# Kernel tuning notes

Hardware: AMD Instinct MI355X
Metric: run time of the kernel (lower is better)

The kernel has to match this reference:

```python
import jax, jax.numpy as jnp
import numpy as np

# ---- configuration (mirrors cfg used by the torch module) ----
H = W = 64          # cfg.KEYPOINT.HEATMAP_SIZE
C = 256             # cfg.KEYPOINT.NFEATS
N = 2               # batch (number of view pairs)
S = 32              # cfg.EPIPOLAR.SAMPLESIZE
DS = 4              # cfg.BACKBONE.DOWNSAMPLE
EPS = 1e-3          # self.epsilon


def pix2coord(v):
    # feature-map pixel -> original-image coordinate
    return v * DS + DS / 2.0 - 0.5


def _camera_pair():
    # realistic stereo pair: image is 256x256 (64x64 heatmap * downsample 4)
    K = np.array([[300.0, 0.0, 127.5], [0.0, 300.0, 127.5], [0.0, 0.0, 1.0]])
    P1 = K @ np.hstack([np.eye(3), np.zeros((3, 1))])
    ang = np.deg2rad(15.0)
    R = np.array([[np.cos(ang), 0, np.sin(ang)], [0, 1, 0], [-np.sin(ang), 0, np.cos(ang)]])
    t = np.array([[-0.5], [0.0], [0.1]])
    P2 = K @ np.hstack([R, t])
    return P1.astype(np.float32), P2.astype(np.float32)


def setup_inputs() -> dict:
    key = jax.random.key(0)
    k1, k2 = jax.random.split(key)
    feat1 = jax.random.normal(k1, (N, C, H, W), dtype=jnp.float32)
    feat2 = jax.random.normal(k2, (N, C, H, W), dtype=jnp.float32)
    P1np, P2np = _camera_pair()
    P1 = jnp.asarray(np.stack([P1np] * N))
    P2 = jnp.asarray(np.stack([P2np] * N))
    return {"feat1": feat1, "feat2": feat2, "P1": P1, "P2": P2}


def _fundamental(P1, P2):
    # F = [e2]_x P2 P1^+ ; camera center = null vector of P1
    P1inv = jnp.linalg.pinv(P1)          # 4x3
    _, _, Vt = jnp.linalg.svd(P1)
    Cc = Vt[-1]                          # homogeneous camera center, (4,)
    e2 = P2 @ Cc                         # epipole in view 2, (3,)
    z = jnp.zeros(())
    skew = jnp.stack([jnp.stack([z, -e2[2], e2[1]]),
                      jnp.stack([e2[2], z, -e2[0]]),
                      jnp.stack([-e2[1], e2[0], z])])
    return skew @ (P2 @ P1inv)


def _sample_locs(P1, P2):
    """Epipolar-line sample locations, [S, N, H, W, 2] normalized to [-1,1]."""
    xs = pix2coord(jnp.arange(W, dtype=jnp.float32))
    ys = pix2coord(jnp.arange(H, dtype=jnp.float32))
    xmin, xmax = xs[0], xs[-1]
    ymin, ymax = ys[0], ys[-1]
    gy, gx = jnp.meshgrid(ys, xs, indexing='ij')
    grid = jnp.stack([gx.ravel(), gy.ravel(), jnp.ones(H * W, jnp.float32)])

    F = jax.vmap(_fundamental)(P1, P2)
    lines = jnp.einsum('nij,jp->nip', F, grid)
    a, b, c = lines[:, 0], lines[:, 1], lines[:, 2]
    a_s = jnp.where(jnp.abs(a) < EPS, EPS, a)
    b_s = jnp.where(jnp.abs(b) < EPS, EPS, b)
    # intersections of a*x + b*y + c = 0 with the 4 image borders
    y_at_xmin = -(c + a * xmin) / b_s
    y_at_xmax = -(c + a * xmax) / b_s
    x_at_ymin = -(c + b * ymin) / a_s
    x_at_ymax = -(c + b * ymax) / a_s
    cx = jnp.stack([jnp.full_like(a, xmin), jnp.full_like(a, xmax), x_at_ymin, x_at_ymax], -1)  # N,HW,4
    cy = jnp.stack([y_at_xmin, y_at_xmax, jnp.full_like(a, ymin), jnp.full_like(a, ymax)], -1)
    tol = 1e-2
    valid = (cx >= xmin - tol) & (cx <= xmax + tol) & (cy >= ymin - tol) & (cy <= ymax + tol)
    # invalid -> far out of range (equivalent of self.outrange_tensor);
    # such sample locs fall outside [-1,1] and contribute zeros in grid_sample
    cx = jnp.where(valid, cx, xmin - 10000.0)
    cy = jnp.where(valid, cy, ymin - 10000.0)
    order = jnp.argsort(jnp.logical_not(valid), axis=-1)  # stable: valid candidates first
    pick = order[..., :2]                                 # N,HW,2
    px = jnp.take_along_axis(cx, pick, axis=-1)
    py = jnp.take_along_axis(cy, pick, axis=-1)
    # normalize original-image coords to [-1,1] over the feature grid extent
    nx = (px - xmin) / (xmax - xmin) * 2.0 - 1.0
    ny = (py - ymin) / (ymax - ymin) * 2.0 - 1.0
    start = jnp.stack([nx[..., 0], ny[..., 0]], -1)       # N,HW,2
    end = jnp.stack([nx[..., 1], ny[..., 1]], -1)
    steps = jnp.linspace(0.0, 1.0, S).reshape(S, 1, 1, 1)
    locs = start[None] + steps * (end - start)[None]      # S,N,HW,2
    return locs.reshape(S, N, H, W, 2)


def _grid_sample(img, grid):
    """Bilinear sampling with zeros padding. img [C,H,W], grid [S,H,W,2] -> [S,C,H,W]."""
    gx, gy = grid[..., 0], grid[..., 1]
    x = (gx + 1.0) * 0.5 * (W - 1)
    y = (gy + 1.0) * 0.5 * (H - 1)
    x0 = jnp.floor(x)
    y0 = jnp.floor(y)
    wx = x - x0
    wy = y - y0
    x0i = x0.astype(jnp.int32)
    y0i = y0.astype(jnp.int32)

    def gather(yi, xi, w):
        inb = (yi >= 0) & (yi <= H - 1) & (xi >= 0) & (xi <= W - 1)
        yc = jnp.clip(yi, 0, H - 1)
        xc = jnp.clip(xi, 0, W - 1)
        vals = img[:, yc, xc]                  # C,S,H,W
        return vals * (w * inb)[None]

    out = (gather(y0i, x0i, (1 - wy) * (1 - wx))
           + gather(y0i, x0i + 1, (1 - wy) * wx)
           + gather(y0i + 1, x0i, wy * (1 - wx))
           + gather(y0i + 1, x0i + 1, wy * wx))
    return out.transpose(1, 0, 2, 3)           # S,C,H,W


def reference(feat1, feat2, P1, P2):
    # geometry (torch.no_grad in original)
    locs = jax.lax.stop_gradient(_sample_locs(P1, P2))   # S,N,H,W,2
    locs_n = jnp.transpose(locs, (1, 0, 2, 3, 4))        # N,S,H,W,2
    sampled = jax.vmap(_grid_sample)(feat2, locs_n)      # N,S,C,H,W
    # dot-product similarity + softmax attention over the epipolar samples ('avg')
    sim = jax.nn.softmax(jnp.einsum('nchw,nschw->nshw', feat1, sampled), axis=1)
    out = jnp.einsum('nshw,nschw->nchw', sim, sampled)   # N,C,H,W
    return out
```

## Files before the change

### kernel.cpp

```cpp
#include <hip/hip_runtime.h>
#include <math.h>

#define H 64
#define W 64
#define C 256
#define NB 2
#define SS 32
#define HW (H*W)

typedef __attribute__((ext_vector_type(2))) _Float16 half2v;

__device__ __forceinline__ half2v pk2(float a) {
  return __builtin_bit_cast(half2v, __builtin_amdgcn_cvt_pkrtz(a, a));
}

__device__ void fmat_compute(const float* __restrict__ P1f,
                             const float* __restrict__ P2f,
                             double* __restrict__ Fout, int n) {
  double p1[3][4], p2[3][4];
  for (int i = 0; i < 3; ++i)
    for (int j = 0; j < 4; ++j) {
      p1[i][j] = (double)P1f[n * 12 + i * 4 + j];
      p2[i][j] = (double)P2f[n * 12 + i * 4 + j];
    }
  double A[3][3];
  for (int i = 0; i < 3; ++i)
    for (int j = 0; j < 3; ++j) {
      double s = 0;
      for (int k = 0; k < 4; ++k) s += p1[i][k] * p1[j][k];
      A[i][j] = s;
    }
  double det = A[0][0] * (A[1][1] * A[2][2] - A[1][2] * A[2][1])
             - A[0][1] * (A[1][0] * A[2][2] - A[1][2] * A[2][0])
             + A[0][2] * (A[1][0] * A[2][1] - A[1][1] * A[2][0]);
  double id = 1.0 / det;
  double Ai[3][3];
  Ai[0][0] = (A[1][1] * A[2][2] - A[1][2] * A[2][1]) * id;
  Ai[0][1] = (A[0][2] * A[2][1] - A[0][1] * A[2][2]) * id;
  Ai[0][2] = (A[0][1] * A[1][2] - A[0][2] * A[1][1]) * id;
  Ai[1][0] = (A[1][2] * A[2][0] - A[1][0] * A[2][2]) * id;
  Ai[1][1] = (A[0][0] * A[2][2] - A[0][2] * A[2][0]) * id;
  Ai[1][2] = (A[0][2] * A[1][0] - A[0][0] * A[1][2]) * id;
  Ai[2][0] = (A[1][0] * A[2][1] - A[1][1] * A[2][0]) * id;
  Ai[2][1] = (A[0][1] * A[2][0] - A[0][0] * A[2][1]) * id;
  Ai[2][2] = (A[0][0] * A[1][1] - A[0][1] * A[1][0]) * id;
  double Pi[4][3];
  for (int i = 0; i < 4; ++i)
    for (int j = 0; j < 3; ++j) {
      double s = 0;
      for (int k = 0; k < 3; ++k) s += p1[k][i] * Ai[k][j];
      Pi[i][j] = s;
    }
  double M[3][3];
  for (int i = 0; i < 3; ++i)
    for (int j = 0; j < 3; ++j) {
      double s = 0;
      for (int k = 0; k < 4; ++k) s += p2[i][k] * Pi[k][j];
      M[i][j] = s;
    }
  double nv[4];
  {
    auto det3 = [&](int ca, int cb, int cc) {
      return p1[0][ca] * (p1[1][cb] * p1[2][cc] - p1[1][cc] * p1[2][cb])
           - p1[0][cb] * (p1[1][ca] * p1[2][cc] - p1[1][cc] * p1[2][ca])
           + p1[0][cc] * (p1[1][ca] * p1[2][cb] - p1[1][cb] * p1[2][ca]);
    };
    nv[0] =  det3(1, 2, 3);
    nv[1] = -det3(0, 2, 3);
    nv[2] =  det3(0, 1, 3);
    nv[3] = -det3(0, 1, 2);
  }
  double nn = sqrt(nv[0]*nv[0] + nv[1]*nv[1] + nv[2]*nv[2] + nv[3]*nv[3]);
  for (int i = 0; i < 4; ++i) nv[i] /= nn;
  double e2[3];
  for (int i = 0; i < 3; ++i) {
    double s = 0;
    for (int j = 0; j < 4; ++j) s += p2[i][j] * nv[j];
    e2[i] = s;
  }
  for (int j = 0; j < 3; ++j) {
    Fout[n * 9 + 0 * 3 + j] = -e2[2] * M[1][j] + e2[1] * M[2][j];
    Fout[n * 9 + 1 * 3 + j] =  e2[2] * M[0][j] - e2[0] * M[2][j];
    Fout[n * 9 + 2 * 3 + j] = -e2[1] * M[0][j] + e2[0] * M[1][j];
  }
}

__global__ __launch_bounds__(256) void prep_kernel(
    const float* __restrict__ feat2,
    const float* __restrict__ P1f, const float* __restrict__ P2f,
    _Float16* __restrict__ f2t, double* __restrict__ Fd) {
  __shared__ float tile[32][33];
  const int n  = blockIdx.z;
  const int p0 = blockIdx.x * 32;
  const int c0 = blockIdx.y * 32;
  const int tx = threadIdx.x, ty = threadIdx.y;
  const float* src = feat2 + (size_t)n * (C * HW);
#pragma unroll
  for (int j = 0; j < 4; ++j) {
    int cc = c0 + ty + j * 8;
    tile[ty + j * 8][tx] = src[(size_t)cc * HW + p0 + tx];
  }
  __syncthreads();
  {
    const int tid = ty * 32 + tx;
    const int pp = tid >> 3;
    const int cp = tid & 7;
    _Float16* dst = f2t + (size_t)n * (HW * C) + (size_t)(p0 + pp) * C + c0;
#pragma unroll
    for (int jj = 0; jj < 2; ++jj) {
      const int cc = (cp + jj * 8) * 2;
      half2v h2;
      h2.x = (_Float16)tile[cc][pp];
      h2.y = (_Float16)tile[cc + 1][pp];
      *(half2v*)(dst + cc) = h2;
    }
  }
  if (n == 0 && blockIdx.x == 0 && blockIdx.y == 0) {
    int t = ty * 32 + tx;
    if (t < NB) fmat_compute(P1f, P2f, Fd, t);
  }
}

__device__ __forceinline__ float groupsum32(float v) {
  v += __int_as_float(__builtin_amdgcn_update_dpp(
         0, __float_as_int(v), 0xB1, 0xF, 0xF, true));
  v += __int_as_float(__builtin_amdgcn_update_dpp(
         0, __float_as_int(v), 0x4E, 0xF, 0xF, true));
  v += __int_as_float(__builtin_amdgcn_update_dpp(
         0, __float_as_int(v), 0x124, 0xF, 0xF, true));
  v += __int_as_float(__builtin_amdgcn_update_dpp(
         0, __float_as_int(v), 0x128, 0xF, 0xF, true));
  v += __int_as_float(__builtin_amdgcn_ds_swizzle(
         __float_as_int(v), 0x401F));
  return v;
}

struct Stage {
  uint4 a, b, c, d;
  half2v wa, wb, wc, wd;
};

__global__ __launch_bounds__(256) void epi_main(
    const float* __restrict__ feat1, const _Float16* __restrict__ f2t,
    const double* __restrict__ Fd, float* __restrict__ out) {
  const int tid  = threadIdx.x;
  const int lane = tid & 63;
  const int wv   = tid >> 6;
  const int grp  = lane >> 5;
  const int cl   = lane & 31;
  const int bid  = blockIdx.x;
  const int r    = bid & 7;
  const int k    = bid >> 3;
  const int n    = r >> 2;
  const int sub  = r & 3;
  const int p    = (sub * 128 + k) * 8 + wv * 2 + grp;
  const int h = p >> 6, w = p & (W - 1);
  const int cb = cl * 8;

  float f1r[8];
  {
    const float* f1b = feat1 + ((size_t)n * C + cb) * HW + p;
#pragma unroll
    for (int i = 0; i < 8; ++i) f1r[i] = f1b[(size_t)i * HW];
  }

  const double* Fdp = Fd + n * 9;
  const float F0 = (float)Fdp[0], F1 = (float)Fdp[1], F2 = (float)Fdp[2];
  const float F3 = (float)Fdp[3], F4 = (float)Fdp[4], F5 = (float)Fdp[5];
  const float F6 = (float)Fdp[6], F7 = (float)Fdp[7], F8 = (float)Fdp[8];
  const float X = w * 4.0f + 1.5f;
  const float Y = h * 4.0f + 1.5f;
  const float a = F0 * X + F1 * Y + F2;
  const float b = F3 * X + F4 * Y + F5;
  const float c = F6 * X + F7 * Y + F8;
  const float a_s = (fabsf(a) < 1e-3f) ? 1e-3f : a;
  const float b_s = (fabsf(b) < 1e-3f) ? 1e-3f : b;
  const float xmin = 1.5f, xmax = 253.5f, ymin = 1.5f, ymax = 253.5f, tol = 0.01f;
  float cx[4], cy[4];
  cx[0] = xmin;  cy[0] = -(c + a * xmin) / b_s;
  cx[1] = xmax;  cy[1] = -(c + a * xmax) / b_s;
  cx[2] = -(c + b * ymin) / a_s;  cy[2] = ymin;
  cx[3] = -(c + b * ymax) / a_s;  cy[3] = ymax;
  bool valid[4];
#pragma unroll
  for (int i = 0; i < 4; ++i)
    valid[i] = (cx[i] >= xmin - tol) && (cx[i] <= xmax + tol) &&
               (cy[i] >= ymin - tol) && (cy[i] <= ymax + tol);
#pragma unroll
  for (int i = 0; i < 4; ++i)
    if (!valid[i]) { cx[i] = xmin - 10000.0f; cy[i] = ymin - 10000.0f; }
  int pk0 = -1, pk1 = -1;
#pragma unroll
  for (int i = 0; i < 4; ++i)
    if (valid[i]) { if (pk0 < 0) pk0 = i; else if (pk1 < 0) pk1 = i; }
#pragma unroll
  for (int i = 0; i < 4; ++i)
    if (!valid[i]) { if (pk0 < 0) pk0 = i; else if (pk1 < 0) pk1 = i; }
  const float x0p = (cx[pk0] - 1.5f) * 0.25f;
  const float y0p = (cy[pk0] - 1.5f) * 0.25f;
  const float pdx = (cx[pk1] - 1.5f) * 0.25f - x0p;
  const float pdy = (cy[pk1] - 1.5f) * 0.25f - y0p;

  const _Float16* f2b = f2t + (size_t)n * HW * C + cb;

  float m = -1e30f, l = 0.f;
  half2v acc2[4];
#pragma unroll
  for (int i = 0; i < 4; ++i) acc2[i] = (half2v)(_Float16)0;

  auto issue = [&](int s, Stage& st) {
    const float t = (float)s * (1.0f / 31.0f);
    const float x = fmaf(t, pdx, x0p);
    const float y = fmaf(t, pdy, y0p);
    const float xf = floorf(x), yf = floorf(y);
    const float wx = x - xf, wy = y - yf;
    const int x0 = (int)xf, y0 = (int)yf;
    const bool bx0 = ((unsigned)x0 < W), bx1 = ((unsigned)(x0 + 1) < W);
    const bool by0 = ((unsigned)y0 < H), by1 = ((unsigned)(y0 + 1) < H);
    const int xc0 = min(max(x0, 0), W - 1);
    const int xc1 = min(max(x0 + 1, 0), W - 1);
    const int yc0 = min(max(y0, 0), H - 1);
    const int yc1 = min(max(y0 + 1, 0), H - 1);
    const float u0 = 1.f - wx, v0 = 1.f - wy;
    const float w00 = v0 * u0 * (float)(bx0 & by0);
    const float w01 = v0 * wx * (float)(bx1 & by0);
    const float w10 = wy * u0 * (float)(bx0 & by1);
    const float w11 = wy * wx * (float)(bx1 & by1);
    st.wa = pk2(w00);
    st.wb = pk2(w01);
    st.wc = pk2(w10);
    st.wd = pk2(w11);
    const int r0 = yc0 * W, r1 = yc1 * W;
    st.a = *(const uint4*)(f2b + (r0 + xc0) * C);
    st.b = *(const uint4*)(f2b + (r0 + xc1) * C);
    st.c = *(const uint4*)(f2b + (r1 + xc0) * C);
    st.d = *(const uint4*)(f2b + (r1 + xc1) * C);
  };

  auto process = [&](const Stage& st) {
    half2v q[4];
    {
      const uint* ap = (const uint*)&st.a;
      const uint* bp = (const uint*)&st.b;
      const uint* cp = (const uint*)&st.c;
      const uint* dp = (const uint*)&st.d;
#pragma unroll
      for (int j = 0; j < 4; ++j) {
        half2v qa = __builtin_bit_cast(half2v, ap[j]) * st.wa;
        qa += __builtin_bit_cast(half2v, bp[j]) * st.wb;
        qa += __builtin_bit_cast(half2v, cp[j]) * st.wc;
        qa += __builtin_bit_cast(half2v, dp[j]) * st.wd;
        q[j] = qa;
      }
    }
    float part = 0.f;
#pragma unroll
    for (int j = 0; j < 4; ++j) {
      part = fmaf(f1r[2 * j],     (float)q[j].x, part);
      part = fmaf(f1r[2 * j + 1], (float)q[j].y, part);
    }
    part = groupsum32(part);

    if (__any(part > m + 4.f)) {
      const float mn = fmaxf(m, part);
      const float sc = __expf(m - mn);
      l *= sc;
      const half2v sch = pk2(sc);
#pragma unroll
      for (int i = 0; i < 4; ++i) acc2[i] *= sch;
      m = mn;
    }
    const float e = __expf(part - m);
    l += e;
    const half2v eh = pk2(e);
#pragma unroll
    for (int i = 0; i < 4; ++i) acc2[i] += eh * q[i];
  };

  Stage sA, sB, sC;
  issue(0, sA);
  issue(1, sB);
  for (int k3 = 0; k3 < 30; k3 += 3) {
    issue(k3 + 2, sC);
    process(sA);
    issue(k3 + 3, sA);
    process(sB);
    issue(k3 + 4, sB);
    process(sC);
  }
  process(sA);
  process(sB);

  const float inv = 1.0f / l;
  float* ob = out + (size_t)n * C * HW + (size_t)cb * HW + p;
#pragma unroll
  for (int i = 0; i < 4; ++i) {
    ob[(size_t)(2 * i) * HW]     = (float)acc2[i].x * inv;
    ob[(size_t)(2 * i + 1) * HW] = (float)acc2[i].y * inv;
  }
}

extern "C" void kernel_launch(void* const* d_in, const int* in_sizes, int n_in,
                              void* d_out, int out_size, void* d_ws, size_t ws_size,
                              hipStream_t stream) {
  const float* feat1 = (const float*)d_in[0];
  const float* feat2 = (const float*)d_in[1];
  const float* P1 = (const float*)d_in[2];
  const float* P2 = (const float*)d_in[3];
  float* out = (float*)d_out;

  char* ws = (char*)d_ws;
  _Float16* f2t = (_Float16*)ws;
  double*   Fd  = (double*)(ws + (5u << 20));

  prep_kernel<<<dim3(HW / 32, C / 32, NB), dim3(32, 8), 0, stream>>>(
      feat2, P1, P2, f2t, Fd);
  epi_main<<<NB * HW / 8, 256, 0, stream>>>(feat1, f2t, Fd, out);
}
```

Before: 40.67 us.

## Use fp16 dot2 for similarity and process samples in unrolled pairs

Feat1 values are packed to fp16 pairs so the similarity dot product can use the packed fdot2 instruction instead of per-element float conversions and FMAs. The explicit three-stage software pipeline is replaced by a fully unrolled loop that handles two samples per step, sharing one online-softmax rescale check and one max per pair. This cuts ALU and cross-lane reduction overhead per sample, but feat1 drops to fp16 precision and prefetch depth is left to the compiler, which may raise register pressure or hide less load latency.

```diff
diff --git a/kernel.cpp b/kernel.cpp
--- a/kernel.cpp
+++ b/kernel.cpp
@@ -9,9 +9,21 @@
 #define HW (H*W)
 
 typedef __attribute__((ext_vector_type(2))) _Float16 half2v;
+typedef __attribute__((ext_vector_type(2))) __fp16   fp16x2;
 
 __device__ __forceinline__ half2v pk2(float a) {
   return __builtin_bit_cast(half2v, __builtin_amdgcn_cvt_pkrtz(a, a));
+}
+
+__device__ __forceinline__ float fdot2(half2v a, half2v b, float c) {
+#if __has_builtin(__builtin_amdgcn_fdot2)
+  return __builtin_amdgcn_fdot2(__builtin_bit_cast(fp16x2, a),
+                                __builtin_bit_cast(fp16x2, b), c, false);
+#else
+  c = fmaf((float)a.x, (float)b.x, c);
+  c = fmaf((float)a.y, (float)b.y, c);
+  return c;
+#endif
 }
 
 __device__ void fmat_compute(const float* __restrict__ P1f,
@@ -134,11 +146,6 @@
          __float_as_int(v), 0x401F));
   return v;
 }
-
-struct Stage {
-  uint4 a, b, c, d;
-  half2v wa, wb, wc, wd;
-};
 
 __global__ __launch_bounds__(256) void epi_main(
     const float* __restrict__ feat1, const _Float16* __restrict__ f2t,
@@ -157,11 +164,15 @@
   const int h = p >> 6, w = p & (W - 1);
   const int cb = cl * 8;
 
-  float f1r[8];
+  half2v f1h[4];
   {
     const float* f1b = feat1 + ((size_t)n * C + cb) * HW + p;
 #pragma unroll
-    for (int i = 0; i < 8; ++i) f1r[i] = f1b[(size_t)i * HW];
+    for (int i = 0; i < 4; ++i) {
+      const float lo = f1b[(size_t)(2 * i) * HW];
+      const float hi = f1b[(size_t)(2 * i + 1) * HW];
+      f1h[i] = __builtin_bit_cast(half2v, __builtin_amdgcn_cvt_pkrtz(lo, hi));
+    }
   }
 
   const double* Fdp = Fd + n * 9;
@@ -208,7 +219,8 @@
 #pragma unroll
   for (int i = 0; i < 4; ++i) acc2[i] = (half2v)(_Float16)0;
 
-  auto issue = [&](int s, Stage& st) {
+  auto fetch = [&](int s, uint4& A, uint4& B, uint4& Cc, uint4& D,
+                   half2v& wa, half2v& wb, half2v& wc, half2v& wd) {
     const float t = (float)s * (1.0f / 31.0f);
     const float x = fmaf(t, pdx, x0p);
     const float y = fmaf(t, pdy, y0p);
@@ -222,47 +234,53 @@
     const int yc0 = min(max(y0, 0), H - 1);
     const int yc1 = min(max(y0 + 1, 0), H - 1);
     const float u0 = 1.f - wx, v0 = 1.f - wy;
-    const float w00 = v0 * u0 * (float)(bx0 & by0);
-    const float w01 = v0 * wx * (float)(bx1 & by0);
-    const float w10 = wy * u0 * (float)(bx0 & by1);
-    const float w11 = wy * wx * (float)(bx1 & by1);
-    st.wa = pk2(w00);
-    st.wb = pk2(w01);
-    st.wc = pk2(w10);
-    st.wd = pk2(w11);
+    wa = pk2(v0 * u0 * (float)(bx0 & by0));
+    wb = pk2(v0 * wx * (float)(bx1 & by0));
+    wc = pk2(wy * u0 * (float)(bx0 & by1));
+    wd = pk2(wy * wx * (float)(bx1 & by1));
     const int r0 = yc0 * W, r1 = yc1 * W;
-    st.a = *(const uint4*)(f2b + (r0 + xc0) * C);
-    st.b = *(const uint4*)(f2b + (r0 + xc1) * C);
-    st.c = *(const uint4*)(f2b + (r1 + xc0) * C);
-    st.d = *(const uint4*)(f2b + (r1 + xc1) * C);
+    A  = *(const uint4*)(f2b + (r0 + xc0) * C);
+    B  = *(const uint4*)(f2b + (r0 + xc1) * C);
+    Cc = *(const uint4*)(f2b + (r1 + xc0) * C);
+    D  = *(const uint4*)(f2b + (r1 + xc1) * C);
   };
 
-  auto process = [&](const Stage& st) {
-    half2v q[4];
-    {
-      const uint* ap = (const uint*)&st.a;
-      const uint* bp = (const uint*)&st.b;
-      const uint* cp = (const uint*)&st.c;
-      const uint* dp = (const uint*)&st.d;
-#pragma unroll
-      for (int j = 0; j < 4; ++j) {
-        half2v qa = __builtin_bit_cast(half2v, ap[j]) * st.wa;
-        qa += __builtin_bit_cast(half2v, bp[j]) * st.wb;
-        qa += __builtin_bit_cast(half2v, cp[j]) * st.wc;
-        qa += __builtin_bit_cast(half2v, dp[j]) * st.wd;
-        q[j] = qa;
-      }
-    }
-    float part = 0.f;
+  auto bilin = [&](const uint4& A, const uint4& B, const uint4& Cc,
+                   const uint4& D, half2v wa, half2v wb, half2v wc, half2v wd,
+                   half2v q[4], float& part) {
+    const uint* ap = (const uint*)&A;
+    const uint* bp = (const uint*)&B;
+    const uint* cp = (const uint*)&Cc;
+    const uint* dp = (const uint*)&D;
+    part = 0.f;
 #pragma unroll
     for (int j = 0; j < 4; ++j) {
-      part = fmaf(f1r[2 * j],     (float)q[j].x, part);
-      part = fmaf(f1r[2 * j + 1], (float)q[j].y, part);
-    }
-    part = groupsum32(part);
-
-    if (__any(part > m + 4.f)) {
-      const float mn = fmaxf(m, part);
+      half2v qa = __builtin_bit_cast(half2v, ap[j]) * wa;
+      qa += __builtin_bit_cast(half2v, bp[j]) * wb;
+      qa += __builtin_bit_cast(half2v, cp[j]) * wc;
+      qa += __builtin_bit_cast(half2v, dp[j]) * wd;
+      q[j] = qa;
+      part = fdot2(qa, f1h[j], part);
+    }
+  };
+
+#pragma unroll
+  for (int s = 0; s < SS; s += 2) {
+    uint4 A0, B0, C0, D0, A1, B1, C1, D1;
+    half2v wa0, wb0, wc0, wd0, wa1, wb1, wc1, wd1;
+    fetch(s,     A0, B0, C0, D0, wa0, wb0, wc0, wd0);
+    fetch(s + 1, A1, B1, C1, D1, wa1, wb1, wc1, wd1);
+
+    half2v q0[4], q1[4];
+    float p0, p1;
+    bilin(A0, B0, C0, D0, wa0, wb0, wc0, wd0, q0, p0);
+    bilin(A1, B1, C1, D1, wa1, wb1, wc1, wd1, q1, p1);
+    p0 = groupsum32(p0);
+    p1 = groupsum32(p1);
+
+    const float mx = fmaxf(p0, p1);
+    if (__any(mx > m + 4.f)) {
+      const float mn = fmaxf(m, mx);
       const float sc = __expf(m - mn);
       l *= sc;
       const half2v sch = pk2(sc);
@@ -270,26 +288,17 @@
       for (int i = 0; i < 4; ++i) acc2[i] *= sch;
       m = mn;
     }
-    const float e = __expf(part - m);
-    l += e;
-    const half2v eh = pk2(e);
-#pragma unroll
-    for (int i = 0; i < 4; ++i) acc2[i] += eh * q[i];
-  };
-
-  Stage sA, sB, sC;
-  issue(0, sA);
-  issue(1, sB);
-  for (int k3 = 0; k3 < 30; k3 += 3) {
-    issue(k3 + 2, sC);
-    process(sA);
-    issue(k3 + 3, sA);
-    process(sB);
-    issue(k3 + 4, sB);
-    process(sC);
-  }
-  process(sA);
-  process(sB);
+    const float e0 = __expf(p0 - m);
+    const float e1 = __expf(p1 - m);
+    l += e0 + e1;
+    const half2v eh0 = pk2(e0);
+    const half2v eh1 = pk2(e1);
+#pragma unroll
+    for (int i = 0; i < 4; ++i) {
+      acc2[i] += eh0 * q0[i];
+      acc2[i] += eh1 * q1[i];
+    }
+  }
 
   const float inv = 1.0f / l;
   float* ob = out + (size_t)n * C * HW + (size_t)cb * HW + p;
```

New measurement: 39.51 us. 2.9% less time.
